# Kernel optimization log

Hardware: AMD Instinct MI355X
Metric: run time of the kernel (lower is better)

Reference implementation:

```python
import jax, jax.numpy as jnp
import numpy as np

N, E, G = 30000, 120000, 256
F_IN, F_E, H, T = 16, 8, 32, 10
EPS = 1e-5


def setup_inputs() -> dict:
    key = jax.random.key(0)
    ks = jax.random.split(key, 16)
    s = 0.05
    inp = {
        'x': jax.random.normal(ks[0], (N, F_IN), jnp.float32),
        'edge_attr': jax.random.normal(ks[1], (E, F_E), jnp.float32),
        'edge_index': jax.random.randint(ks[2], (2, E), 0, N),
        'batch': jnp.sort(jax.random.randint(ks[3], (N,), 0, G)),
        'c1_nn_w': jax.random.normal(ks[4], (F_E, F_IN * H), jnp.float32) * s,
        'c1_nn_b': jnp.zeros((F_IN * H,), jnp.float32),
        'c1_root': jax.random.normal(ks[5], (F_IN, H), jnp.float32) * s,
        'c1_bias': jnp.zeros((H,), jnp.float32),
        'c2_nn_w': jax.random.normal(ks[6], (F_E, H * H), jnp.float32) * s,
        'c2_nn_b': jnp.zeros((H * H,), jnp.float32),
        'c2_root': jax.random.normal(ks[7], (H, H), jnp.float32) * s,
        'c2_bias': jnp.zeros((H,), jnp.float32),
        'c3_nn_w': jax.random.normal(ks[8], (F_E, H * H), jnp.float32) * s,
        'c3_nn_b': jnp.zeros((H * H,), jnp.float32),
        'c3_root': jax.random.normal(ks[9], (H, H), jnp.float32) * s,
        'c3_bias': jnp.zeros((H,), jnp.float32),
        'bn1_g': jnp.ones((H,), jnp.float32), 'bn1_b': jnp.zeros((H,), jnp.float32),
        'bn1_m': jnp.zeros((H,), jnp.float32), 'bn1_v': jnp.ones((H,), jnp.float32),
        'bn2_g': jnp.ones((H,), jnp.float32), 'bn2_b': jnp.zeros((H,), jnp.float32),
        'bn2_m': jnp.zeros((H,), jnp.float32), 'bn2_v': jnp.ones((H,), jnp.float32),
        'mlp_w1': jax.random.normal(ks[10], (H, H), jnp.float32) * s,
        'mlp_b1': jnp.zeros((H,), jnp.float32),
        'mlp_w2': jax.random.normal(ks[11], (H, T), jnp.float32) * s,
        'mlp_b2': jnp.zeros((T,), jnp.float32),
    }
    return inp


def _nnconv(x, edge_index, edge_attr, nn_w, nn_b, root, bias, in_dim, out_dim):
    # per-edge weight matrix from edge features: [E, in_dim, out_dim]
    W = (edge_attr @ nn_w + nn_b).reshape(-1, in_dim, out_dim)
    # gather source node features, per-edge matvec, scatter-add to targets
    msg = jnp.einsum('ei,eio->eo', x[edge_index[0]], W)
    agg = jax.ops.segment_sum(msg, edge_index[1], num_segments=N)
    return agg + x @ root + bias


def _graph_size_norm(x, batch):
    deg = jax.ops.segment_sum(jnp.ones((N,), x.dtype), batch, num_segments=G)
    inv_sqrt = jnp.where(deg > 0, deg, 1.0) ** -0.5
    return x * inv_sqrt[batch][:, None]


def _bn_eval(x, g, b, m, v):
    return (x - m) * (g * jax.lax.rsqrt(v + EPS)) + b


def reference(x, edge_attr, edge_index, batch,
              c1_nn_w, c1_nn_b, c1_root, c1_bias,
              c2_nn_w, c2_nn_b, c2_root, c2_bias,
              c3_nn_w, c3_nn_b, c3_root, c3_bias,
              bn1_g, bn1_b, bn1_m, bn1_v,
              bn2_g, bn2_b, bn2_m, bn2_v,
              mlp_w1, mlp_b1, mlp_w2, mlp_b2):
    h = _nnconv(x, edge_index, edge_attr, c1_nn_w, c1_nn_b, c1_root, c1_bias, F_IN, H)
    h = _graph_size_norm(h, batch)
    h = jax.nn.relu(_bn_eval(h, bn1_g, bn1_b, bn1_m, bn1_v))
    h = _nnconv(h, edge_index, edge_attr, c2_nn_w, c2_nn_b, c2_root, c2_bias, H, H)
    h = _graph_size_norm(h, batch)
    h = jax.nn.relu(_bn_eval(h, bn2_g, bn2_b, bn2_m, bn2_v))
    h = _nnconv(h, edge_index, edge_attr, c3_nn_w, c3_nn_b, c3_root, c3_bias, H, H)
    # global mean pool over graphs
    cnt = jax.ops.segment_sum(jnp.ones((N,), h.dtype), batch, num_segments=G)
    pooled = jax.ops.segment_sum(h, batch, num_segments=G) / jnp.maximum(cnt, 1.0)[:, None]
    # MLP head (dropout inactive in eval)
    out = jax.nn.relu(pooled @ mlp_w1 + mlp_b1) @ mlp_w2 + mlp_b2
    return out
```

## Files before the change

kernel.cpp:

```cpp
#include <hip/hip_runtime.h>

#define NN 30000
#define NE 120000
#define NG 256
#define FIN 16
#define HD 32
#define TOUT 10
#define EPSV 1e-5f
#define NB_SCAN 30

__device__ __forceinline__ void atomAddF(float* p, float v) {
    unsafeAtomicAdd(p, v);
}

__global__ __launch_bounds__(256) void count_deg_kernel(
    const int* __restrict__ eidx, const int* __restrict__ batch,
    int* __restrict__ deg_in, float* __restrict__ deg_g)
{
    const int t = blockIdx.x * 256 + threadIdx.x;
    if (t < NE) atomicAdd(&deg_in[eidx[NE + t]], 1);

    const int lane = threadIdx.x & 63;
    const int g = (t < NN) ? batch[t] : -1;
    const int prev = __shfl_up(g, 1);
    const bool head = (lane == 0) || (g != prev);
    const unsigned long long heads = __ballot(head);
    if (head && g >= 0) {
        unsigned long long higher = (lane < 63) ? (heads >> (lane + 1)) : 0ULL;
        int next = higher ? (lane + __ffsll(higher)) : 64;
        atomAddF(&deg_g[g], (float)(next - lane));
    }
}

__global__ __launch_bounds__(1024) void scan_phase1(
    const int* __restrict__ deg_in, int* __restrict__ row_start,
    int* __restrict__ blocksum)
{
    __shared__ int wsum[16];
    const int t = threadIdx.x, lane = t & 63, w = t >> 6;
    const int idx = blockIdx.x * 1024 + t;
    const int v = (idx < NN) ? deg_in[idx] : 0;
    int s = v;
    #pragma unroll
    for (int off = 1; off < 64; off <<= 1) {
        int u = __shfl_up(s, off, 64);
        if (lane >= off) s += u;
    }
    if (lane == 63) wsum[w] = s;
    __syncthreads();
    if (w == 0) {
        int ws = (lane < 16) ? wsum[lane] : 0;
        #pragma unroll
        for (int off = 1; off < 16; off <<= 1) {
            int u = __shfl_up(ws, off, 64);
            if (lane >= off) ws += u;
        }
        if (lane < 16) wsum[lane] = ws;
    }
    __syncthreads();
    const int incl = s + ((w > 0) ? wsum[w - 1] : 0);
    if (idx < NN) row_start[idx] = incl - v;
    if (t == 1023) blocksum[blockIdx.x] = incl;
}

__global__ __launch_bounds__(64) void scan_phase2(
    const int* __restrict__ blocksum, int* __restrict__ blockoff)
{
    const int t = threadIdx.x;
    const int v = (t < NB_SCAN) ? blocksum[t] : 0;
    int s = v;
    #pragma unroll
    for (int off = 1; off < 64; off <<= 1) {
        int u = __shfl_up(s, off, 64);
        if (t >= off) s += u;
    }
    if (t < NB_SCAN) blockoff[t] = s - v;
}

__global__ __launch_bounds__(1024) void scan_phase3(
    const int* __restrict__ blockoff, int* __restrict__ row_start,
    int* __restrict__ cursor)
{
    const int idx = blockIdx.x * 1024 + threadIdx.x;
    if (idx < NN) {
        const int r = row_start[idx] + blockoff[blockIdx.x];
        row_start[idx] = r;
        cursor[idx]    = r;
    }
    if (blockIdx.x == 0 && threadIdx.x == 0) row_start[NN] = NE;
}

__global__ __launch_bounds__(256) void csr_scatter(
    const int* __restrict__ eidx, int* __restrict__ cursor,
    int2* __restrict__ csr)
{
    const int e = blockIdx.x * 256 + threadIdx.x;
    if (e < NE) {
        const int d = eidx[NE + e];
        const int slot = atomicAdd(&cursor[d], 1);
        csr[slot] = make_int2(e, eidx[e]);
    }
}

template<int IN, bool FINAL>
__global__ __launch_bounds__(256) void fused_layer(
    const float* __restrict__ hin,
    const float* __restrict__ ea,
    const int2*  __restrict__ csr,
    const int*   __restrict__ row_start,
    const float* __restrict__ nn_w,
    const float* __restrict__ nn_b,
    const float* __restrict__ root,
    const float* __restrict__ bias,
    const int*   __restrict__ batch,
    const float* __restrict__ deg_g,
    const float* __restrict__ bn_g,
    const float* __restrict__ bn_b,
    const float* __restrict__ bn_m,
    const float* __restrict__ bn_v,
    float*       __restrict__ out)
{
    constexpr int WTOT = 10 * IN * 32;
    constexpr int NQ2  = 32 / IN;
    __shared__ float Wl[WTOT];
    __shared__ float Ts[4][2][10][IN];

    const int tid = threadIdx.x;
    const int wv  = tid >> 6;
    const int l   = tid & 63;
    const int l5  = l & 31;
    const int pr  = l >> 5;
    const int i   = l5 & (IN - 1);
    const int q   = l5 / IN;
    const int o   = l5;

    for (int idx = tid; idx < WTOT; idx += 256) {
        const int row = idx / (IN * 32);
        const int r   = idx % (IN * 32);
        const int i4  = r >> 7;
        const int rr  = r & 127;
        const int oo  = rr >> 2;
        const int il  = rr & 3;
        const int ii  = i4 * 4 + il;
        const float* src = (row < 8) ? (nn_w + row * (IN * 32))
                                     : (row == 8 ? nn_b : root);
        Wl[idx] = src[ii * 32 + oo];
    }
    __syncthreads();

    #pragma unroll
    for (int j = 0; j < 2; ++j) {
        const int d = blockIdx.x * 16 + j * 8 + wv * 2 + pr;

        float t[9];
        #pragma unroll
        for (int f = 0; f < 9; ++f) t[f] = 0.0f;

        const int p0 = row_start[d];
        const int p1 = row_start[d + 1];

        int p = p0 + q;
        int2 es = (p < p1) ? csr[p] : make_int2(0, 0);
        float  xv = hin[(long)es.y * IN + i];
        float4 a  = *(const float4*)(ea + (long)es.x * 8);
        float4 b  = *(const float4*)(ea + (long)es.x * 8 + 4);

        while (p < p1) {
            const int pn = p + NQ2;
            const int2 esn = (pn < p1) ? csr[pn] : make_int2(0, 0);
            const float  xvn = hin[(long)esn.y * IN + i];
            const float4 an  = *(const float4*)(ea + (long)esn.x * 8);
            const float4 bn  = *(const float4*)(ea + (long)esn.x * 8 + 4);

            t[0] = fmaf(a.x, xv, t[0]);
            t[1] = fmaf(a.y, xv, t[1]);
            t[2] = fmaf(a.z, xv, t[2]);
            t[3] = fmaf(a.w, xv, t[3]);
            t[4] = fmaf(b.x, xv, t[4]);
            t[5] = fmaf(b.y, xv, t[5]);
            t[6] = fmaf(b.z, xv, t[6]);
            t[7] = fmaf(b.w, xv, t[7]);
            t[8] += xv;

            p = pn; es = esn; xv = xvn; a = an; b = bn;
        }

        if (IN == 16) {
            #pragma unroll
            for (int f = 0; f < 9; ++f) t[f] += __shfl_xor(t[f], 16, 64);
        }

        __builtin_amdgcn_wave_barrier();
        if (l5 < IN) {
            #pragma unroll
            for (int f = 0; f < 9; ++f) Ts[wv][pr][f][i] = t[f];
            Ts[wv][pr][9][i] = hin[(long)d * IN + i];
        }
        __builtin_amdgcn_wave_barrier();

        float acc = bias[o];
        #pragma unroll
        for (int row = 0; row < 10; ++row) {
            const float* wrow = Wl + row * (IN * 32);
            #pragma unroll
            for (int i4 = 0; i4 < IN / 4; ++i4) {
                const float4 w4 = *(const float4*)(wrow + i4 * 128 + (o << 2));
                const float4 tv = *(const float4*)(&Ts[wv][pr][row][i4 << 2]);
                acc = fmaf(tv.x, w4.x, acc);
                acc = fmaf(tv.y, w4.y, acc);
                acc = fmaf(tv.z, w4.z, acc);
                acc = fmaf(tv.w, w4.w, acc);
            }
        }

        const int g = batch[d];
        if (!FINAL) {
            float dg = deg_g[g];
            dg = dg > 0.0f ? dg : 1.0f;
            float v = acc * (1.0f / sqrtf(dg));
            const float s = bn_g[o] / sqrtf(bn_v[o] + EPSV);
            v = (v - bn_m[o]) * s + bn_b[o];
            out[(long)d * 32 + o] = v > 0.0f ? v : 0.0f;
        } else {
            float v = acc;
            const int   g2 = __shfl(g, l ^ 32, 64);
            const float v2 = __shfl(v, l ^ 32, 64);
            bool do_store = true;
            if (g2 == g) {
                if (l & 32) do_store = false;
                else        v += v2;
            }
            if (do_store) atomAddF(&out[g * 32 + o], v);
        }
    }
}

__global__ __launch_bounds__(64) void head_kernel(
    const float* __restrict__ pooled,
    const float* __restrict__ deg,
    const float* __restrict__ w1,
    const float* __restrict__ b1,
    const float* __restrict__ w2,
    const float* __restrict__ b2,
    float*       __restrict__ out)
{
    const int g = blockIdx.x * 64 + threadIdx.x;
    if (g >= NG) return;
    float cnt = deg[g];
    cnt = cnt > 1.0f ? cnt : 1.0f;

    float p[HD];
    #pragma unroll
    for (int i = 0; i < HD; ++i) p[i] = pooled[g * HD + i] / cnt;

    float hid[HD];
    #pragma unroll
    for (int j = 0; j < HD; ++j) {
        float a = b1[j];
        #pragma unroll
        for (int i = 0; i < HD; ++i)
            a = fmaf(p[i], w1[i * HD + j], a);
        hid[j] = a > 0.0f ? a : 0.0f;
    }
    #pragma unroll
    for (int t = 0; t < TOUT; ++t) {
        float a = b2[t];
        #pragma unroll
        for (int j = 0; j < HD; ++j)
            a = fmaf(hid[j], w2[j * TOUT + t], a);
        out[g * TOUT + t] = a;
    }
}

extern "C" void kernel_launch(void* const* d_in, const int* in_sizes, int n_in,
                              void* d_out, int out_size, void* d_ws, size_t ws_size,
                              hipStream_t stream)
{
    const float* x        = (const float*)d_in[0];
    const float* ea       = (const float*)d_in[1];
    const int*   eidx     = (const int*)  d_in[2];
    const int*   batch    = (const int*)  d_in[3];
    const float* c1_nn_w  = (const float*)d_in[4];
    const float* c1_nn_b  = (const float*)d_in[5];
    const float* c1_root  = (const float*)d_in[6];
    const float* c1_bias  = (const float*)d_in[7];
    const float* c2_nn_w  = (const float*)d_in[8];
    const float* c2_nn_b  = (const float*)d_in[9];
    const float* c2_root  = (const float*)d_in[10];
    const float* c2_bias  = (const float*)d_in[11];
    const float* c3_nn_w  = (const float*)d_in[12];
    const float* c3_nn_b  = (const float*)d_in[13];
    const float* c3_root  = (const float*)d_in[14];
    const float* c3_bias  = (const float*)d_in[15];
    const float* bn1_g    = (const float*)d_in[16];
    const float* bn1_b    = (const float*)d_in[17];
    const float* bn1_m    = (const float*)d_in[18];
    const float* bn1_v    = (const float*)d_in[19];
    const float* bn2_g    = (const float*)d_in[20];
    const float* bn2_b    = (const float*)d_in[21];
    const float* bn2_m    = (const float*)d_in[22];
    const float* bn2_v    = (const float*)d_in[23];
    const float* mlp_w1   = (const float*)d_in[24];
    const float* mlp_b1   = (const float*)d_in[25];
    const float* mlp_w2   = (const float*)d_in[26];
    const float* mlp_b2   = (const float*)d_in[27];
    float* out = (float*)d_out;

    float* h1     = (float*)d_ws;
    float* h2     = h1 + NN * HD;
    float* deg_g  = h2 + NN * HD;
    float* pooled = deg_g + NG;
    int*   ibase  = (int*)(pooled + NG * HD);
    int2*  csr    = (int2*)ibase;
    int*   deg_in = ibase + 2 * NE;
    int*   row_s  = deg_in + NN;
    int*   cursor = row_s + NN + 1;
    int*   bsum   = cursor + NN;
    int*   boff   = bsum + NB_SCAN;

    hipMemsetAsync(deg_in, 0, sizeof(int) * NN, stream);
    hipMemsetAsync(deg_g,  0, sizeof(float) * (NG + NG * HD), stream);

    const int egrid = (NE + 255) / 256;

    count_deg_kernel<<<egrid, 256, 0, stream>>>(eidx, batch, deg_in, deg_g);
    scan_phase1<<<NB_SCAN, 1024, 0, stream>>>(deg_in, row_s, bsum);
    scan_phase2<<<1, 64, 0, stream>>>(bsum, boff);
    scan_phase3<<<NB_SCAN, 1024, 0, stream>>>(boff, row_s, cursor);
    csr_scatter<<<egrid, 256, 0, stream>>>(eidx, cursor, csr);

    const int lgrid = NN / 16;

    fused_layer<FIN, false><<<lgrid, 256, 0, stream>>>(
        x, ea, csr, row_s, c1_nn_w, c1_nn_b, c1_root, c1_bias,
        batch, deg_g, bn1_g, bn1_b, bn1_m, bn1_v, h1);

    fused_layer<HD, false><<<lgrid, 256, 0, stream>>>(
        h1, ea, csr, row_s, c2_nn_w, c2_nn_b, c2_root, c2_bias,
        batch, deg_g, bn2_g, bn2_b, bn2_m, bn2_v, h2);

    fused_layer<HD, true><<<lgrid, 256, 0, stream>>>(
        h2, ea, csr, row_s, c3_nn_w, c3_nn_b, c3_root, c3_bias,
        batch, deg_g, nullptr, nullptr, nullptr, nullptr, pooled);

    head_kernel<<<(NG + 63) / 64, 64, 0, stream>>>(pooled, deg_g, mlp_w1, mlp_b1,
                                                   mlp_w2, mlp_b2, out);
}
```

Measured before the change: 266.4 us.

## Build CSR in one single-block kernel and keep layer weights in registers

Result: slower. 626.2 us (+135.0%).

```diff
diff --git a/kernel.cpp b/kernel.cpp
--- a/kernel.cpp
+++ b/kernel.cpp
@@ -7,98 +7,89 @@
 #define HD 32
 #define TOUT 10
 #define EPSV 1e-5f
-#define NB_SCAN 30
 
 __device__ __forceinline__ void atomAddF(float* p, float v) {
     unsafeAtomicAdd(p, v);
 }
 
-__global__ __launch_bounds__(256) void count_deg_kernel(
+__global__ __launch_bounds__(1024) void build_csr(
     const int* __restrict__ eidx, const int* __restrict__ batch,
-    int* __restrict__ deg_in, float* __restrict__ deg_g)
+    int*  __restrict__ row_start,
+    int*  __restrict__ cursor,
+    int2* __restrict__ csr,
+    float* __restrict__ deg_g)
 {
-    const int t = blockIdx.x * 256 + threadIdx.x;
-    if (t < NE) atomicAdd(&deg_in[eidx[NE + t]], 1);
-
-    const int lane = threadIdx.x & 63;
-    const int g = (t < NN) ? batch[t] : -1;
-    const int prev = __shfl_up(g, 1);
-    const bool head = (lane == 0) || (g != prev);
-    const unsigned long long heads = __ballot(head);
-    if (head && g >= 0) {
-        unsigned long long higher = (lane < 63) ? (heads >> (lane + 1)) : 0ULL;
-        int next = higher ? (lane + __ffsll(higher)) : 64;
-        atomAddF(&deg_g[g], (float)(next - lane));
-    }
-}
-
-__global__ __launch_bounds__(1024) void scan_phase1(
-    const int* __restrict__ deg_in, int* __restrict__ row_start,
-    int* __restrict__ blocksum)
-{
+    __shared__ int packed[NN / 2];
     __shared__ int wsum[16];
+    __shared__ int carry_s;
+
     const int t = threadIdx.x, lane = t & 63, w = t >> 6;
-    const int idx = blockIdx.x * 1024 + t;
-    const int v = (idx < NN) ? deg_in[idx] : 0;
-    int s = v;
-    #pragma unroll
-    for (int off = 1; off < 64; off <<= 1) {
-        int u = __shfl_up(s, off, 64);
-        if (lane >= off) s += u;
-    }
-    if (lane == 63) wsum[w] = s;
-    __syncthreads();
-    if (w == 0) {
-        int ws = (lane < 16) ? wsum[lane] : 0;
-        #pragma unroll
-        for (int off = 1; off < 16; off <<= 1) {
-            int u = __shfl_up(ws, off, 64);
-            if (lane >= off) ws += u;
-        }
-        if (lane < 16) wsum[lane] = ws;
-    }
-    __syncthreads();
-    const int incl = s + ((w > 0) ? wsum[w - 1] : 0);
-    if (idx < NN) row_start[idx] = incl - v;
-    if (t == 1023) blocksum[blockIdx.x] = incl;
-}
-
-__global__ __launch_bounds__(64) void scan_phase2(
-    const int* __restrict__ blocksum, int* __restrict__ blockoff)
-{
-    const int t = threadIdx.x;
-    const int v = (t < NB_SCAN) ? blocksum[t] : 0;
-    int s = v;
-    #pragma unroll
-    for (int off = 1; off < 64; off <<= 1) {
-        int u = __shfl_up(s, off, 64);
-        if (t >= off) s += u;
-    }
-    if (t < NB_SCAN) blockoff[t] = s - v;
-}
-
-__global__ __launch_bounds__(1024) void scan_phase3(
-    const int* __restrict__ blockoff, int* __restrict__ row_start,
-    int* __restrict__ cursor)
-{
-    const int idx = blockIdx.x * 1024 + threadIdx.x;
-    if (idx < NN) {
-        const int r = row_start[idx] + blockoff[blockIdx.x];
-        row_start[idx] = r;
-        cursor[idx]    = r;
-    }
-    if (blockIdx.x == 0 && threadIdx.x == 0) row_start[NN] = NE;
-}
-
-__global__ __launch_bounds__(256) void csr_scatter(
-    const int* __restrict__ eidx, int* __restrict__ cursor,
-    int2* __restrict__ csr)
-{
-    const int e = blockIdx.x * 256 + threadIdx.x;
-    if (e < NE) {
+
+    for (int ii = t; ii < NN / 2; ii += 1024) packed[ii] = 0;
+    if (t == 0) carry_s = 0;
+    __syncthreads();
+
+    for (int e = t; e < NE; e += 1024) {
+        const int d = eidx[NE + e];
+        atomicAdd(&packed[d >> 1], 1 << ((d & 1) << 4));
+    }
+    __syncthreads();
+
+    for (int base = 0; base < NN / 2; base += 1024) {
+        const int idx = base + t;
+        const int pv = (idx < NN / 2) ? packed[idx] : 0;
+        const int lo = pv & 0xffff;
+        const int v  = lo + (pv >> 16);
+        int s = v;
+        #pragma unroll
+        for (int off = 1; off < 64; off <<= 1) {
+            const int u = __shfl_up(s, off, 64);
+            if (lane >= off) s += u;
+        }
+        if (lane == 63) wsum[w] = s;
+        __syncthreads();
+        if (w == 0) {
+            int ws = (lane < 16) ? wsum[lane] : 0;
+            #pragma unroll
+            for (int off = 1; off < 16; off <<= 1) {
+                const int u = __shfl_up(ws, off, 64);
+                if (lane >= off) ws += u;
+            }
+            if (lane < 16) wsum[lane] = ws;
+        }
+        __syncthreads();
+        const int incl  = s + ((w > 0) ? wsum[w - 1] : 0);
+        const int carry = carry_s;
+        if (idx < NN / 2) {
+            const int excl = carry + incl - v;
+            *(int2*)(row_start + 2 * idx) = make_int2(excl, excl + lo);
+            *(int2*)(cursor    + 2 * idx) = make_int2(excl, excl + lo);
+        }
+        __syncthreads();
+        if (t == 1023) carry_s += incl;
+        __syncthreads();
+    }
+    if (t == 0) row_start[NN] = NE;
+    __syncthreads();
+
+    for (int e = t; e < NE; e += 1024) {
         const int d = eidx[NE + e];
         const int slot = atomicAdd(&cursor[d], 1);
         csr[slot] = make_int2(e, eidx[e]);
+    }
+
+    for (int base = 0; base < NN; base += 1024) {
+        const int n = base + t;
+        const int g = (n < NN) ? batch[n] : -1;
+        const int prev = __shfl_up(g, 1);
+        const bool head = (lane == 0) || (g != prev);
+        const unsigned long long heads = __ballot(head);
+        if (head && g >= 0) {
+            const unsigned long long higher =
+                (lane < 63) ? (heads >> (lane + 1)) : 0ULL;
+            const int next = higher ? (lane + __ffsll(higher)) : 64;
+            atomAddF(&deg_g[g], (float)(next - lane));
+        }
     }
 }
 
@@ -120,37 +111,40 @@
     const float* __restrict__ bn_v,
     float*       __restrict__ out)
 {
-    constexpr int WTOT = 10 * IN * 32;
-    constexpr int NQ2  = 32 / IN;
-    __shared__ float Wl[WTOT];
-    __shared__ float Ts[4][2][10][IN];
+    constexpr int K  = 10 * IN;
+    constexpr int KQ = K / 4;
+    constexpr int KL = KQ / 2;
+    constexpr int NQ = 32 / IN;
+
+    __shared__ float Tlds[16 * K];
+    __shared__ float P[4 * 16 * 64];
 
     const int tid = threadIdx.x;
     const int wv  = tid >> 6;
     const int l   = tid & 63;
+    const int h   = l >> 5;
+    const int o   = l & 31;
     const int l5  = l & 31;
     const int pr  = l >> 5;
-    const int i   = l5 & (IN - 1);
-    const int q   = l5 / IN;
-    const int o   = l5;
-
-    for (int idx = tid; idx < WTOT; idx += 256) {
-        const int row = idx / (IN * 32);
-        const int r   = idx % (IN * 32);
-        const int i4  = r >> 7;
-        const int rr  = r & 127;
-        const int oo  = rr >> 2;
-        const int il  = rr & 3;
-        const int ii  = i4 * 4 + il;
-        const float* src = (row < 8) ? (nn_w + row * (IN * 32))
-                                     : (row == 8 ? nn_b : root);
-        Wl[idx] = src[ii * 32 + oo];
-    }
-    __syncthreads();
+
+    float Wreg[KL];
+    const int kbase = wv * KQ + h * KL;
+    #pragma unroll
+    for (int kk = 0; kk < KL; ++kk) {
+        const int k = kbase + kk;
+        const float* src = (k < 8 * IN) ? (nn_w + k * 32)
+                         : (k < 9 * IN) ? (nn_b + (k - 8 * IN) * 32)
+                                        : (root + (k - 9 * IN) * 32);
+        Wreg[kk] = src[o];
+    }
+
+    const int i = l5 & (IN - 1);
+    const int q = l5 / IN;
 
     #pragma unroll
     for (int j = 0; j < 2; ++j) {
-        const int d = blockIdx.x * 16 + j * 8 + wv * 2 + pr;
+        const int nloc = wv * 4 + j * 2 + pr;
+        const int d    = blockIdx.x * 16 + nloc;
 
         float t[9];
         #pragma unroll
@@ -166,7 +160,7 @@
         float4 b  = *(const float4*)(ea + (long)es.x * 8 + 4);
 
         while (p < p1) {
-            const int pn = p + NQ2;
+            const int pn = p + NQ;
             const int2 esn = (pn < p1) ? csr[pn] : make_int2(0, 0);
             const float  xvn = hin[(long)esn.y * IN + i];
             const float4 an  = *(const float4*)(ea + (long)esn.x * 8);
@@ -190,47 +184,60 @@
             for (int f = 0; f < 9; ++f) t[f] += __shfl_xor(t[f], 16, 64);
         }
 
-        __builtin_amdgcn_wave_barrier();
         if (l5 < IN) {
+            float* tb = Tlds + nloc * K;
             #pragma unroll
-            for (int f = 0; f < 9; ++f) Ts[wv][pr][f][i] = t[f];
-            Ts[wv][pr][9][i] = hin[(long)d * IN + i];
-        }
-        __builtin_amdgcn_wave_barrier();
-
-        float acc = bias[o];
-        #pragma unroll
-        for (int row = 0; row < 10; ++row) {
-            const float* wrow = Wl + row * (IN * 32);
-            #pragma unroll
-            for (int i4 = 0; i4 < IN / 4; ++i4) {
-                const float4 w4 = *(const float4*)(wrow + i4 * 128 + (o << 2));
-                const float4 tv = *(const float4*)(&Ts[wv][pr][row][i4 << 2]);
-                acc = fmaf(tv.x, w4.x, acc);
-                acc = fmaf(tv.y, w4.y, acc);
-                acc = fmaf(tv.z, w4.z, acc);
-                acc = fmaf(tv.w, w4.w, acc);
-            }
-        }
-
+            for (int f = 0; f < 9; ++f) tb[f * IN + i] = t[f];
+            tb[9 * IN + i] = hin[(long)d * IN + i];
+        }
+    }
+    __syncthreads();
+
+    for (int n = 0; n < 16; ++n) {
+        const float* tb = Tlds + n * K + kbase;
+        float acc = 0.0f;
+        #pragma unroll
+        for (int kq = 0; kq < KL / 4; ++kq) {
+            const float4 tv = *(const float4*)(tb + kq * 4);
+            acc = fmaf(Wreg[4 * kq + 0], tv.x, acc);
+            acc = fmaf(Wreg[4 * kq + 1], tv.y, acc);
+            acc = fmaf(Wreg[4 * kq + 2], tv.z, acc);
+            acc = fmaf(Wreg[4 * kq + 3], tv.w, acc);
+        }
+        P[(wv * 16 + n) * 64 + l] = acc;
+    }
+    __syncthreads();
+
+    #pragma unroll
+    for (int r = 0; r < 2; ++r) {
+        const int idx = r * 256 + tid;
+        const int n   = idx >> 5;
+        const int oo  = idx & 31;
+        float sum = bias[oo];
+        #pragma unroll
+        for (int ww = 0; ww < 4; ++ww) {
+            const float* pb = P + (ww * 16 + n) * 64;
+            sum += pb[oo] + pb[32 + oo];
+        }
+        const int d = blockIdx.x * 16 + n;
         const int g = batch[d];
         if (!FINAL) {
             float dg = deg_g[g];
             dg = dg > 0.0f ? dg : 1.0f;
-            float v = acc * (1.0f / sqrtf(dg));
-            const float s = bn_g[o] / sqrtf(bn_v[o] + EPSV);
-            v = (v - bn_m[o]) * s + bn_b[o];
-            out[(long)d * 32 + o] = v > 0.0f ? v : 0.0f;
+            float v = sum * (1.0f / sqrtf(dg));
+            const float s = bn_g[oo] / sqrtf(bn_v[oo] + EPSV);
+            v = (v - bn_m[oo]) * s + bn_b[oo];
+            out[(long)d * 32 + oo] = v > 0.0f ? v : 0.0f;
         } else {
-            float v = acc;
-            const int   g2 = __shfl(g, l ^ 32, 64);
-            const float v2 = __shfl(v, l ^ 32, 64);
+            float v = sum;
+            const int   g2 = __shfl(g, (tid & 63) ^ 32, 64);
+            const float v2 = __shfl(v, (tid & 63) ^ 32, 64);
             bool do_store = true;
             if (g2 == g) {
-                if (l & 32) do_store = false;
-                else        v += v2;
+                if (tid & 32) do_store = false;
+                else          v += v2;
             }
-            if (do_store) atomAddF(&out[g * 32 + o], v);
+            if (do_store) atomAddF(&out[g * 32 + oo], v);
         }
     }
 }
@@ -312,22 +319,12 @@
     float* pooled = deg_g + NG;
     int*   ibase  = (int*)(pooled + NG * HD);
     int2*  csr    = (int2*)ibase;
-    int*   deg_in = ibase + 2 * NE;
-    int*   row_s  = deg_in + NN;
-    int*   cursor = row_s + NN + 1;
-    int*   bsum   = cursor + NN;
-    int*   boff   = bsum + NB_SCAN;
-
-    hipMemsetAsync(deg_in, 0, sizeof(int) * NN, stream);
-    hipMemsetAsync(deg_g,  0, sizeof(float) * (NG + NG * HD), stream);
-
-    const int egrid = (NE + 255) / 256;
-
-    count_deg_kernel<<<egrid, 256, 0, stream>>>(eidx, batch, deg_in, deg_g);
-    scan_phase1<<<NB_SCAN, 1024, 0, stream>>>(deg_in, row_s, bsum);
-    scan_phase2<<<1, 64, 0, stream>>>(bsum, boff);
-    scan_phase3<<<NB_SCAN, 1024, 0, stream>>>(boff, row_s, cursor);
-    csr_scatter<<<egrid, 256, 0, stream>>>(eidx, cursor, csr);
+    int*   row_s  = ibase + 2 * NE;
+    int*   cursor = row_s + NN + 2;
+
+    hipMemsetAsync(deg_g, 0, sizeof(float) * (NG + NG * HD), stream);
+
+    build_csr<<<1, 1024, 0, stream>>>(eidx, batch, row_s, cursor, csr, deg_g);
 
     const int lgrid = NN / 16;
 
```
